# Optimization experiments

Measured on AMD Instinct MI355X. Metric: run time of the kernel, lower is better.

The kernel has to match this reference:

```python
import jax, jax.numpy as jnp
import numpy as np

EPS = 1e-7
BURN_IN = 3
INNER_STEPS = 2
N_FEAT, N_TARGET, N_LATENT = 262144, 8192, 32


def setup_inputs() -> dict:
    key = jax.random.key(0)
    ks = jax.random.split(key, 8)
    x = jax.random.normal(ks[0], (N_FEAT,), jnp.float32)
    y = jax.random.normal(ks[1], (N_TARGET,), jnp.float32)
    mu_x = jnp.zeros((N_FEAT,), jnp.float32)
    mu_y = jnp.zeros((N_TARGET,), jnp.float32)
    u0 = jax.random.normal(ks[2], (N_LATENT,), jnp.float32)
    u = u0 / jnp.sqrt(jnp.sum(u0 ** 2))
    Wz = jax.random.normal(ks[3], (N_LATENT, N_FEAT), jnp.float32) * 0.1
    Cz = jax.random.normal(ks[4], (N_LATENT, N_TARGET), jnp.float32) * 0.1
    t_sq_sum = jax.random.uniform(ks[5], (N_LATENT,), jnp.float32) + 1.0
    bz = jax.random.normal(ks[6], (N_LATENT,), jnp.float32) * 0.1
    P = jax.random.normal(ks[7], (N_LATENT, N_FEAT), jnp.float32) * 0.1
    return dict(x=x, y=y, mu_x=mu_x, mu_y=mu_y, u=u, Wz=Wz, Cz=Cz,
                t_sq_sum=t_sq_sum, bz=bz, P=P, n=100)


def _partial_fit(x, y, mu_x, mu_y, u, Wz, Cz, t_sq_sum, bz, P, n):
    # n is a static Python int (sample count before this call)
    n_new = n + 1  # torch: self.n[:] = self.n + 1
    mu_x = (mu_x * n_new + x) / (n_new + 1)
    mu_y = (mu_y * n_new + y) / (n_new + 1)
    xc = x - mu_x
    yc = y - mu_y
    if n_new <= BURN_IN:
        # vectorized burn-in update; only Wz and t_sq_sum change
        Wz = Wz + xc[None, :] * u[:, None]
        tz = Wz @ xc / (jnp.sqrt(jnp.sum(Wz ** 2, axis=1)) + EPS)
        t_sq_sum = t_sq_sum + tz * tz
        return mu_x, mu_y, u, Wz, Cz, t_sq_sum, bz, P

    def comp_step(carry, comp):
        xr, yr = carry
        Wz_i, Cz_i, P_i, u_i, tss, bz_i = comp
        # inner power-iteration refinements (total INNER_STEPS passes)
        for _ in range(INNER_STEPS):
            wz = Wz_i + xr * u_i                                  # [n_feat]
            tz = xr @ wz / (jnp.sqrt(jnp.sum(wz ** 2)) + EPS)     # scalar
            tss_ = tss + tz * tz
            t = tz / jnp.sqrt(tss_)
            cz = Cz_i + yr * t                                    # [n_target]
            C_i = cz / jnp.sqrt(jnp.sum(cz ** 2))
            u_i = yr @ C_i
        bz_new = bz_i + u_i * tz
        b = bz_new / jnp.sqrt(tss_)
        P_new = P_i + xr * t
        xr2 = xr - t * P_new  # deflate x
        yr2 = yr - b * t * C_i  # deflate y
        return (xr2, yr2), (wz, cz, P_new, u_i, tss_, bz_new)

    (_, _), (Wz_n, Cz_n, P_n, u_n, tss_n, bz_n) = jax.lax.scan(
        comp_step, (xc, yc), (Wz, Cz, P, u, t_sq_sum, bz))
    return mu_x, mu_y, u_n, Wz_n, Cz_n, tss_n, bz_n, P_n


def reference(x, y, mu_x, mu_y, u, Wz, Cz, t_sq_sum, bz, P, n):
    outs = _partial_fit(x, y, mu_x, mu_y, u, Wz, Cz, t_sq_sum, bz, P, n)
    # concatenate updated state (mu_x, mu_y, u, Wz, Cz, t_sq_sum, bz, P)
    return jnp.concatenate([o.ravel() for o in outs])
```

## Files before the change

### kernel.cpp

```cpp
#include <hip/hip_runtime.h>


#define NF 262144
#define NT 8192
#define NL 32
#define GYS 36
#define LDSW 260

#define NBX 512
#define KS  512
#define CHK 128
#define NCHK (KS/CHK)
#define GXW 68
#define PBE 2276
#define DIAG 2244

#define WS_PART 0
#define WS_GY   (NBX*PBE)
#define WS_GX   (WS_GY + GYS*GYS)
#define WS_COEF (WS_GX + PBE)

#define OUT_MU_X 0
#define OUT_MU_Y 262144
#define OUT_U    270336
#define OUT_WZ   270368
#define OUT_CZ   8658976
#define OUT_TSS  8921120
#define OUT_BZ   8921152
#define OUT_P    8921184

typedef __attribute__((ext_vector_type(8))) short bf16x8;
typedef __attribute__((ext_vector_type(4))) float f32x4;

__device__ __forceinline__ float4 ld4(const float* p) { return *(const float4*)p; }

__device__ __forceinline__ unsigned int f2bf_rne(float f) {
  unsigned int t = __float_as_uint(f);
  t += 0x7FFFu + ((t >> 16) & 1u);
  return t >> 16;
}

__device__ __forceinline__ double rsq64(double x) {
  double r = __builtin_amdgcn_rsq(x);
  r = r * (1.5 - 0.5 * x * r * r);
  return r;
}

__global__ __launch_bounds__(320) void gram_kernel(
    const float* __restrict__ x, const float* __restrict__ y,
    const float* __restrict__ mux, const float* __restrict__ muy,
    const float* __restrict__ Wz, const float* __restrict__ Cz,
    const float* __restrict__ P, const int* __restrict__ np,
    float* __restrict__ ws)
{
  __shared__ __align__(16) char smem[80 * CHK * 4 + 128];
  const int tid = threadIdx.x;
  const int b = blockIdx.x;
  const float n1 = (float)(np[0] + 1);
  const float cmu = n1 / (n1 + 1.0f);

  if (b < NBX) {
    char* hB = smem;
    char* lB = smem + 80 * CHK * 2;
    float* sdiag = (float*)(smem + 80 * CHK * 4);

    if (tid < 32) sdiag[tid] = 0.f;
    {
      unsigned int* hz = (unsigned int*)hB;
      unsigned int* lz = (unsigned int*)lB;
      for (int i = tid; i < 960; i += 320) { hz[65 * 64 + i] = 0u; lz[65 * 64 + i] = 0u; }
    }

    f32x4 acc0 = {0.f, 0.f, 0.f, 0.f};
    f32x4 acc1 = acc0, acc2 = acc0;
    const int lane = tid & 63;
    const int w = tid >> 6;
    const int col16 = lane & 15;
    const int kgrp = lane >> 4;
    const int swz = (col16 & 7) << 4;

    float4 v[7]; float4 vm0;

    auto issue_loads = [&](int c) {
      const int kb = b * KS + c * CHK;
#pragma unroll
      for (int it = 0; it < 7; ++it) {
        int idx = tid + it * 320;
        if (idx < 2080) {
          int row = idx >> 5;
          int c4 = idx & 31;
          int k = kb + c4 * 4;
          const float* bp = (row == 0) ? (x + k)
                          : (row < 33) ? (P + (size_t)(row - 1) * NF + k)
                                       : (Wz + (size_t)(row - 33) * NF + k);
          v[it] = ld4(bp);
          if (it == 0 && row == 0) vm0 = ld4(mux + k);
        }
      }
    };

    auto convert_write = [&]() {
#pragma unroll
      for (int it = 0; it < 7; ++it) {
        int idx = tid + it * 320;
        if (idx < 2080) {
          int row = idx >> 5;
          int c4 = idx & 31;
          float4 t4 = v[it];
          if (it == 0 && row == 0) {
            t4.x = cmu * (t4.x - vm0.x); t4.y = cmu * (t4.y - vm0.y);
            t4.z = cmu * (t4.z - vm0.z); t4.w = cmu * (t4.w - vm0.w);
          }
          if (row >= 33)
            atomicAdd(&sdiag[row - 33],
                      t4.x * t4.x + t4.y * t4.y + t4.z * t4.z + t4.w * t4.w);
          unsigned int b0 = __float_as_uint(t4.x), b1 = __float_as_uint(t4.y);
          unsigned int b2 = __float_as_uint(t4.z), b3 = __float_as_uint(t4.w);
          float h0 = __uint_as_float(b0 & 0xFFFF0000u);
          float h1 = __uint_as_float(b1 & 0xFFFF0000u);
          float h2 = __uint_as_float(b2 & 0xFFFF0000u);
          float h3 = __uint_as_float(b3 & 0xFFFF0000u);
          uint2 hw, lw;
          hw.x = (b0 >> 16) | ((b1 >> 16) << 16);
          hw.y = (b2 >> 16) | ((b3 >> 16) << 16);
          lw.x = f2bf_rne(t4.x - h0) | (f2bf_rne(t4.y - h1) << 16);
          lw.y = f2bf_rne(t4.z - h2) | (f2bf_rne(t4.w - h3) << 16);
          int off = ((row << 8) + (c4 << 3)) ^ ((row & 7) << 4);
          *(uint2*)(hB + off) = hw;
          *(uint2*)(lB + off) = lw;
        }
      }
    };

    issue_loads(0);
    for (int c = 0; c < NCHK; ++c) {
      __syncthreads();
      convert_write();
      __syncthreads();
      if (c + 1 < NCHK) issue_loads(c + 1);
#pragma unroll
      for (int s = 0; s < 4; ++s) {
        const int kbyte = s * 64 + kgrp * 16;
        const int oa = ((col16 << 8) + kbyte) ^ swz;
        const int ob = oa + (w << 12);
        bf16x8 bh = *(const bf16x8*)(hB + ob);
        bf16x8 bl = *(const bf16x8*)(lB + ob);
        bf16x8 a0h = *(const bf16x8*)(hB + oa);
        bf16x8 a0l = *(const bf16x8*)(lB + oa);
        acc0 = __builtin_amdgcn_mfma_f32_16x16x32_bf16(a0h, bh, acc0, 0, 0, 0);
        acc0 = __builtin_amdgcn_mfma_f32_16x16x32_bf16(a0h, bl, acc0, 0, 0, 0);
        acc0 = __builtin_amdgcn_mfma_f32_16x16x32_bf16(a0l, bh, acc0, 0, 0, 0);
        acc0 = __builtin_amdgcn_mfma_f32_16x16x32_bf16(a0l, bl, acc0, 0, 0, 0);
        bf16x8 a1h = *(const bf16x8*)(hB + oa + 4096);
        bf16x8 a1l = *(const bf16x8*)(lB + oa + 4096);
        acc1 = __builtin_amdgcn_mfma_f32_16x16x32_bf16(a1h, bh, acc1, 0, 0, 0);
        acc1 = __builtin_amdgcn_mfma_f32_16x16x32_bf16(a1h, bl, acc1, 0, 0, 0);
        acc1 = __builtin_amdgcn_mfma_f32_16x16x32_bf16(a1l, bh, acc1, 0, 0, 0);
        acc1 = __builtin_amdgcn_mfma_f32_16x16x32_bf16(a1l, bl, acc1, 0, 0, 0);
        bf16x8 a2h = *(const bf16x8*)(hB + oa + 8192);
        bf16x8 a2l = *(const bf16x8*)(lB + oa + 8192);
        acc2 = __builtin_amdgcn_mfma_f32_16x16x32_bf16(a2h, bh, acc2, 0, 0, 0);
        acc2 = __builtin_amdgcn_mfma_f32_16x16x32_bf16(a2h, bl, acc2, 0, 0, 0);
        acc2 = __builtin_amdgcn_mfma_f32_16x16x32_bf16(a2l, bh, acc2, 0, 0, 0);
        acc2 = __builtin_amdgcn_mfma_f32_16x16x32_bf16(a2l, bl, acc2, 0, 0, 0);
      }
    }
    float* PB = ws + WS_PART + (size_t)b * PBE;
    const int vcol = w * 16 + col16;
    if (vcol < 65) {
#pragma unroll
      for (int r2 = 0; r2 < 4; ++r2) {
        int u = kgrp * 4 + r2;
        PB[u * GXW + vcol] = acc0[r2];
        PB[(16 + u) * GXW + vcol] = acc1[r2];
      }
      if (kgrp == 0) PB[32 * GXW + vcol] = acc2[0];
    }
    if (tid < 32) PB[DIAG + tid] = sdiag[tid];
  } else {
    float* lds = (float*)smem;
    float* GY = ws + WS_GY;
    const int yb = b - NBX;
    int gu = 0, gv = 0; bool active = (tid < 45);
    if (active) {
      int pp = tid;
      for (int g = 0; g < 9; ++g) {
        int cnt = 9 - g;
        if (pp < cnt) { gu = g; gv = g + pp; break; }
        pp -= cnt;
      }
    }
    float acc[16];
#pragma unroll
    for (int i = 0; i < 16; ++i) acc[i] = 0.f;
    const int wb = yb * 256;
    float4 vy[8]; float4 vmy;
#pragma unroll
    for (int it = 0; it < 8; ++it) {
      int idx = tid + it * 320;
      if (idx < 2304) {
        int row = idx >> 6;
        int c4 = idx & 63;
        int k = wb + c4 * 4;
        if (row == 0) {
          vy[it] = ld4(y + k);
          if (it == 0) vmy = ld4(muy + k);
        } else if (row < 33) {
          vy[it] = ld4(Cz + (size_t)(row - 1) * NT + k);
        } else {
          vy[it] = make_float4(0.f, 0.f, 0.f, 0.f);
        }
      }
    }
#pragma unroll
    for (int it = 0; it < 8; ++it) {
      int idx = tid + it * 320;
      if (idx < 2304) {
        int row = idx >> 6;
        int c4 = idx & 63;
        float4 t4 = vy[it];
        if (it == 0 && row == 0) {
          t4.x = cmu * (t4.x - vmy.x); t4.y = cmu * (t4.y - vmy.y);
          t4.z = cmu * (t4.z - vmy.z); t4.w = cmu * (t4.w - vmy.w);
        }
        *(float4*)&lds[row * LDSW + c4 * 4] = t4;
      }
    }
    __syncthreads();
    if (active) {
      const int ub = 4 * gu * LDSW, vb = 4 * gv * LDSW;
      for (int c = 0; c < 64; ++c) {
        float4 av[4], bv[4];
#pragma unroll
        for (int r = 0; r < 4; ++r) av[r] = *(const float4*)&lds[ub + r * LDSW + c * 4];
#pragma unroll
        for (int s = 0; s < 4; ++s) bv[s] = *(const float4*)&lds[vb + s * LDSW + c * 4];
#pragma unroll
        for (int r = 0; r < 4; ++r)
#pragma unroll
          for (int s = 0; s < 4; ++s)
            acc[r * 4 + s] += av[r].x * bv[s].x + av[r].y * bv[s].y +
                              av[r].z * bv[s].z + av[r].w * bv[s].w;
      }
#pragma unroll
      for (int r = 0; r < 4; ++r)
#pragma unroll
        for (int s = 0; s < 4; ++s) {
          int u = 4 * gu + r, v = 4 * gv + s;
          if (u < 33 && v < 33) {
            float val = acc[r * 4 + s];
            atomicAdd(&GY[u * GYS + v], val);
            if (gu != gv) atomicAdd(&GY[v * GYS + u], val);
          }
        }
    }
  }
}

__global__ __launch_bounds__(256) void reduce_kernel(float* __restrict__ ws) {
  const int e = (blockIdx.x % 9) * 256 + threadIdx.x;
  const int c = blockIdx.x / 9;
  if (e < PBE) {
    const float* PB = ws + WS_PART + (size_t)(c * 64) * PBE + e;
    float s0 = 0.f, s1 = 0.f, s2 = 0.f, s3 = 0.f;
#pragma unroll
    for (int j = 0; j < 64; j += 4) {
      s0 += PB[(size_t)j * PBE];
      s1 += PB[(size_t)(j + 1) * PBE];
      s2 += PB[(size_t)(j + 2) * PBE];
      s3 += PB[(size_t)(j + 3) * PBE];
    }
    atomicAdd(ws + WS_GX + e, (s0 + s1) + (s2 + s3));
  }
}

__global__ void solve_kernel(const float* __restrict__ ws,
                             const float* __restrict__ u_in,
                             const float* __restrict__ tss_in,
                             const float* __restrict__ bz_in,
                             float* __restrict__ coef,
                             float* __restrict__ out)
{
  const int l = threadIdx.x;
  const float* GX = ws + WS_GX;
  const float* GY = ws + WS_GY;
  float* AWZT = coef;
  float* APT  = coef + 33 * NL;
  float* ACZT = coef + 66 * NL;

  float rP[32], rW[32], rC[32];
#pragma unroll
  for (int i = 0; i < 32; ++i) rP[i] = GX[(1 + i) * GXW + 1 + l];
#pragma unroll
  for (int i = 0; i < 32; ++i) rW[i] = (l < 32) ? GX[(1 + i) * GXW + 33 + l] : 0.f;
#pragma unroll
  for (int i = 0; i < 32; ++i) rC[i] = GY[(1 + i) * GYS + 1 + l];
  float dS  = (l < 32) ? GX[DIAG + l] : 0.f;
  float u0l = (l < 32) ? u_in[l]   : 0.f;
  float t0l = (l < 32) ? tss_in[l] : 0.f;
  float b0l = (l < 32) ? bz_in[l]  : 0.f;

  double q = (double)GX[0];
  double r = (double)GY[0];
  double pj = (l < 32) ? (double)GX[1 + l]  : 0.0;
  double wj = (l < 32) ? (double)GX[33 + l] : 0.0;
  double ej = (l < 32) ? (double)GY[1 + l]  : 0.0;
  double cx = (l == 0) ? 1.0 : 0.0;
  double cy = (l == 0) ? 1.0 : 0.0;

#pragma unroll
  for (int i = 0; i < NL; ++i) {
    double a  = __shfl(wj, i, 64);
    double g  = __shfl(ej, i, 64);
    double pi = __shfl(pj, i, 64);
    double s  = (double)__shfl(dS, i, 64);
    double h  = (double)__shfl(rC[i], i, 64);
    double Pd = (double)__shfl(rP[i], i, 64);
    double u0   = (double)__shfl(u0l, i, 64);
    double tss0 = (double)__shfl(t0l, i, 64);
    double bz0  = (double)__shfl(b0l, i, 64);

    double ui = u0, u1 = 0.0, tz = 0.0, tss_ = 0.0, t = 0.0;
    double rt = 0.0, rn = 0.0;
#pragma unroll
    for (int pass = 0; pass < 2; ++pass) {
      double num = a + ui * q;
      double s2  = s + 2.0 * ui * a + ui * ui * q;
      double rs  = rsq64(s2);
      tz = num * rs * (1.0 - 1e-7 * rs);
      tss_ = tss0 + tz * tz;
      rt = rsq64(tss_);
      t  = tz * rt;
      double ncz2 = h + 2.0 * t * g + t * t * r;
      rn = rsq64(ncz2);
      ui = (g + t * r) * rn;
      if (pass == 0) u1 = ui;
    }
    double u2 = ui;
    double bz_new = bz0 + u2 * tz;
    double bb = bz_new * rt;
    double phi = 1.0 - t * t;
    double gam = bb * t * rn;
    double psi = 1.0 - gam * t;

    if (l == 0) {
      out[OUT_U + i]   = (float)u2;
      out[OUT_TSS + i] = (float)tss_;
      out[OUT_BZ + i]  = (float)bz_new;
    }
    if (l < 33) {
      AWZT[l * 32 + i] = (float)(u1 * cx);
      APT [l * 32 + i] = (float)(t  * cx) + ((l == 1 + i) ? 1.0f : 0.0f);
      ACZT[l * 32 + i] = (float)(t  * cy) + ((l == 1 + i) ? 1.0f : 0.0f);
    }
    q = phi * phi * q - 2.0 * phi * t * pi + t * t * Pd;
    r = psi * psi * r - 2.0 * psi * gam * g + gam * gam * h;
    cx *= phi; if (l == 1 + i) cx -= t;
    cy *= psi; if (l == 1 + i) cy -= gam;
    if (l < 32) {
      pj = phi * pj - t * (double)rP[i];
      wj = phi * wj - t * (double)rW[i];
      ej = psi * ej - gam * (double)rC[i];
    }
  }
}

__global__ __launch_bounds__(256) void out_kernel(
    const float* __restrict__ x, const float* __restrict__ y,
    const float* __restrict__ mux, const float* __restrict__ muy,
    const float* __restrict__ Wz, const float* __restrict__ Cz,
    const float* __restrict__ P, const int* __restrict__ np,
    const float* __restrict__ coef, float* __restrict__ out)
{
  const int b = blockIdx.x, tid = threadIdx.x;
  const float n1 = (float)(np[0] + 1);
  const float inv = 1.0f / (n1 + 1.0f);
  const float* AWZT = coef;
  const float* APT  = coef + 33 * NL;
  const float* ACZT = coef + 66 * NL;

  if (b < 1024) {
    const int k = b * 256 + tid;
    float xv = x[k], mv = mux[k];
    float mn = (mv * n1 + xv) * inv;
    out[OUT_MU_X + k] = mn;
    float accW[32], accP[32];
#pragma unroll
    for (int i = 0; i < 32; ++i) accW[i] = Wz[(size_t)i * NF + k];
#pragma unroll
    for (int i = 0; i < 32; ++i) accP[i] = 0.f;
    {
      float B0 = xv - mn;
#pragma unroll
      for (int i = 0; i < 32; ++i) {
        accW[i] += AWZT[i] * B0;
        accP[i] += APT[i] * B0;
      }
    }
#pragma unroll 4
    for (int j = 1; j < 33; ++j) {
      float Bj = P[(size_t)(j - 1) * NF + k];
      const float* cw = AWZT + j * 32;
      const float* cp = APT + j * 32;
#pragma unroll
      for (int i = 0; i < 32; ++i) {
        accW[i] += cw[i] * Bj;
        accP[i] += cp[i] * Bj;
      }
    }
#pragma unroll
    for (int i = 0; i < 32; ++i) out[OUT_WZ + (size_t)i * NF + k] = accW[i];
#pragma unroll
    for (int i = 0; i < 32; ++i) out[OUT_P + (size_t)i * NF + k] = accP[i];
  } else {
    const int k = (b - 1024) * 256 + tid;
    float yv = y[k], mv = muy[k];
    float mn = (mv * n1 + yv) * inv;
    out[OUT_MU_Y + k] = mn;
    float accC[32];
#pragma unroll
    for (int i = 0; i < 32; ++i) accC[i] = 0.f;
    {
      float B0 = yv - mn;
#pragma unroll
      for (int i = 0; i < 32; ++i) accC[i] += ACZT[i] * B0;
    }
#pragma unroll 4
    for (int j = 1; j < 33; ++j) {
      float Bj = Cz[(size_t)(j - 1) * NT + k];
      const float* cc = ACZT + j * 32;
#pragma unroll
      for (int i = 0; i < 32; ++i) accC[i] += cc[i] * Bj;
    }
#pragma unroll
    for (int i = 0; i < 32; ++i) out[OUT_CZ + (size_t)i * NT + k] = accC[i];
  }
}

extern "C" void kernel_launch(void* const* d_in, const int* in_sizes, int n_in,
                              void* d_out, int out_size, void* d_ws, size_t ws_size,
                              hipStream_t stream) {
  const float* x   = (const float*)d_in[0];
  const float* y   = (const float*)d_in[1];
  const float* mux = (const float*)d_in[2];
  const float* muy = (const float*)d_in[3];
  const float* u   = (const float*)d_in[4];
  const float* Wz  = (const float*)d_in[5];
  const float* Cz  = (const float*)d_in[6];
  const float* tss = (const float*)d_in[7];
  const float* bz  = (const float*)d_in[8];
  const float* P   = (const float*)d_in[9];
  const int*   n   = (const int*)d_in[10];
  float* ws  = (float*)d_ws;
  float* out = (float*)d_out;

  hipMemsetAsync(ws + WS_GY, 0, (size_t)(GYS * GYS + PBE) * sizeof(float), stream);
  gram_kernel<<<NBX + 32, 320, 0, stream>>>(x, y, mux, muy, Wz, Cz, P, n, ws);
  reduce_kernel<<<72, 256, 0, stream>>>(ws);
  solve_kernel<<<1, 64, 0, stream>>>(ws, u, tss, bz, ws + WS_COEF, out);
  out_kernel<<<1024 + 32, 256, 0, stream>>>(x, y, mux, muy, Wz, Cz, P, n, ws + WS_COEF, out);
}
```

Before: 233.1 us.

## Double the gram grid, prefetch both chunks, accumulate partials into atomic slots

The gram kernel now launches twice as many blocks, each covering half the K range. Each block loads both of its chunks up front into two register buffers, so the second load is in flight during the first convert and MFMA pass. Partial Gram results go into 128 shared slots through global atomics instead of one slot per block, which shrinks the reduce kernel's input and needs a larger memset. The per-row diagonal sums now use wave shuffles plus global atomics instead of LDS atomics; the cost is more register pressure and atomic contention on the slots.

```diff
diff --git a/kernel.cpp b/kernel.cpp
--- a/kernel.cpp
+++ b/kernel.cpp
@@ -7,16 +7,17 @@
 #define GYS 36
 #define LDSW 260
 
-#define NBX 512
-#define KS  512
+#define NBX 1024
+#define KS  256
 #define CHK 128
-#define NCHK (KS/CHK)
+#define NCHK 2
+#define NSLOT 128
 #define GXW 68
 #define PBE 2276
 #define DIAG 2244
 
 #define WS_PART 0
-#define WS_GY   (NBX*PBE)
+#define WS_GY   (NSLOT*PBE)
 #define WS_GX   (WS_GY + GYS*GYS)
 #define WS_COEF (WS_GX + PBE)
 
@@ -62,9 +63,8 @@
   if (b < NBX) {
     char* hB = smem;
     char* lB = smem + 80 * CHK * 2;
-    float* sdiag = (float*)(smem + 80 * CHK * 4);
-
-    if (tid < 32) sdiag[tid] = 0.f;
+    float* PB = ws + WS_PART + (size_t)(b & (NSLOT - 1)) * PBE;
+
     {
       unsigned int* hz = (unsigned int*)hB;
       unsigned int* lz = (unsigned int*)lB;
@@ -79,9 +79,9 @@
     const int kgrp = lane >> 4;
     const int swz = (col16 & 7) << 4;
 
-    float4 v[7]; float4 vm0;
-
-    auto issue_loads = [&](int c) {
+    float4 vA[7], vB[7]; float4 vmA, vmB;
+
+    auto issue = [&](int c, float4* v, float4& vm) {
       const int kb = b * KS + c * CHK;
 #pragma unroll
       for (int it = 0; it < 7; ++it) {
@@ -94,12 +94,12 @@
                           : (row < 33) ? (P + (size_t)(row - 1) * NF + k)
                                        : (Wz + (size_t)(row - 33) * NF + k);
           v[it] = ld4(bp);
-          if (it == 0 && row == 0) vm0 = ld4(mux + k);
+          if (it == 0 && row == 0) vm = ld4(mux + k);
         }
       }
     };
 
-    auto convert_write = [&]() {
+    auto convert_write = [&](float4* v, float4& vm) {
 #pragma unroll
       for (int it = 0; it < 7; ++it) {
         int idx = tid + it * 320;
@@ -108,12 +108,18 @@
           int c4 = idx & 31;
           float4 t4 = v[it];
           if (it == 0 && row == 0) {
-            t4.x = cmu * (t4.x - vm0.x); t4.y = cmu * (t4.y - vm0.y);
-            t4.z = cmu * (t4.z - vm0.z); t4.w = cmu * (t4.w - vm0.w);
+            t4.x = cmu * (t4.x - vm.x); t4.y = cmu * (t4.y - vm.y);
+            t4.z = cmu * (t4.z - vm.z); t4.w = cmu * (t4.w - vm.w);
           }
-          if (row >= 33)
-            atomicAdd(&sdiag[row - 33],
-                      t4.x * t4.x + t4.y * t4.y + t4.z * t4.z + t4.w * t4.w);
+          if (row >= 33) {
+            float sq = t4.x * t4.x + t4.y * t4.y + t4.z * t4.z + t4.w * t4.w;
+            sq += __shfl_xor(sq, 1, 64);
+            sq += __shfl_xor(sq, 2, 64);
+            sq += __shfl_xor(sq, 4, 64);
+            sq += __shfl_xor(sq, 8, 64);
+            sq += __shfl_xor(sq, 16, 64);
+            if ((tid & 31) == 0) atomicAdd(&PB[DIAG + row - 33], sq);
+          }
           unsigned int b0 = __float_as_uint(t4.x), b1 = __float_as_uint(t4.y);
           unsigned int b2 = __float_as_uint(t4.z), b3 = __float_as_uint(t4.w);
           float h0 = __uint_as_float(b0 & 0xFFFF0000u);
@@ -132,12 +138,7 @@
       }
     };
 
-    issue_loads(0);
-    for (int c = 0; c < NCHK; ++c) {
-      __syncthreads();
-      convert_write();
-      __syncthreads();
-      if (c + 1 < NCHK) issue_loads(c + 1);
+    auto compute_chunk = [&]() {
 #pragma unroll
       for (int s = 0; s < 4; ++s) {
         const int kbyte = s * 64 + kgrp * 16;
@@ -164,19 +165,28 @@
         acc2 = __builtin_amdgcn_mfma_f32_16x16x32_bf16(a2l, bh, acc2, 0, 0, 0);
         acc2 = __builtin_amdgcn_mfma_f32_16x16x32_bf16(a2l, bl, acc2, 0, 0, 0);
       }
-    }
-    float* PB = ws + WS_PART + (size_t)b * PBE;
+    };
+
+    issue(0, vA, vmA);
+    issue(1, vB, vmB);
+    convert_write(vA, vmA);
+    __syncthreads();
+    compute_chunk();
+    __syncthreads();
+    convert_write(vB, vmB);
+    __syncthreads();
+    compute_chunk();
+
     const int vcol = w * 16 + col16;
     if (vcol < 65) {
 #pragma unroll
       for (int r2 = 0; r2 < 4; ++r2) {
         int u = kgrp * 4 + r2;
-        PB[u * GXW + vcol] = acc0[r2];
-        PB[(16 + u) * GXW + vcol] = acc1[r2];
-      }
-      if (kgrp == 0) PB[32 * GXW + vcol] = acc2[0];
-    }
-    if (tid < 32) PB[DIAG + tid] = sdiag[tid];
+        atomicAdd(&PB[u * GXW + vcol], acc0[r2]);
+        atomicAdd(&PB[(16 + u) * GXW + vcol], acc1[r2]);
+      }
+      if (kgrp == 0) atomicAdd(&PB[32 * GXW + vcol], acc2[0]);
+    }
   } else {
     float* lds = (float*)smem;
     float* GY = ws + WS_GY;
@@ -261,10 +271,10 @@
   const int e = (blockIdx.x % 9) * 256 + threadIdx.x;
   const int c = blockIdx.x / 9;
   if (e < PBE) {
-    const float* PB = ws + WS_PART + (size_t)(c * 64) * PBE + e;
+    const float* PB = ws + WS_PART + (size_t)(c * 32) * PBE + e;
     float s0 = 0.f, s1 = 0.f, s2 = 0.f, s3 = 0.f;
 #pragma unroll
-    for (int j = 0; j < 64; j += 4) {
+    for (int j = 0; j < 32; j += 4) {
       s0 += PB[(size_t)j * PBE];
       s1 += PB[(size_t)(j + 1) * PBE];
       s2 += PB[(size_t)(j + 2) * PBE];
@@ -454,9 +464,9 @@
   float* ws  = (float*)d_ws;
   float* out = (float*)d_out;
 
-  hipMemsetAsync(ws + WS_GY, 0, (size_t)(GYS * GYS + PBE) * sizeof(float), stream);
+  hipMemsetAsync(ws, 0, (size_t)(NSLOT * PBE + GYS * GYS + PBE) * sizeof(float), stream);
   gram_kernel<<<NBX + 32, 320, 0, stream>>>(x, y, mux, muy, Wz, Cz, P, n, ws);
-  reduce_kernel<<<72, 256, 0, stream>>>(ws);
+  reduce_kernel<<<36, 256, 0, stream>>>(ws);
   solve_kernel<<<1, 64, 0, stream>>>(ws, u, tss, bz, ws + WS_COEF, out);
   out_kernel<<<1024 + 32, 256, 0, stream>>>(x, y, mux, muy, Wz, Cz, P, n, ws + WS_COEF, out);
 }
```

Measured after the change: 228.1 us. 2.1% less time.
